# Kernel optimization log

Hardware: AMD Instinct MI355X
Metric: run time of the kernel (lower is better)

## Reference

```python
import jax, jax.numpy as jnp
import numpy as np

D_MODEL = 1024
N_HEADS = 16
HEAD_DIM = D_MODEL // N_HEADS


def setup_inputs() -> dict:
    key = jax.random.key(0)
    k_x, k_q, k_k, k_v = jax.random.split(key, 4)
    B, S = 2, 2048
    x = jax.random.normal(k_x, (B, S, D_MODEL), dtype=jnp.float32)
    # nn.Linear weights stored as [out, in]; we apply x @ W.T
    scale = 1.0 / np.sqrt(D_MODEL)
    W_q = jax.random.uniform(k_q, (D_MODEL, D_MODEL), jnp.float32, -scale, scale)
    W_k = jax.random.uniform(k_k, (D_MODEL, D_MODEL), jnp.float32, -scale, scale)
    W_v = jax.random.uniform(k_v, (D_MODEL, D_MODEL), jnp.float32, -scale, scale)
    return {"x": x, "W_q": W_q, "W_k": W_k, "W_v": W_v}


def reference(x, W_q, W_k, W_v):
    B, S, D = x.shape
    H, Hd = N_HEADS, HEAD_DIM
    # QKV projections (Linear with no bias): x @ W.T
    Q = (x @ W_q.T).reshape(B, S, H, Hd).transpose(0, 2, 1, 3)  # [B,H,S,Hd]
    K = (x @ W_k.T).reshape(B, S, H, Hd).transpose(0, 2, 1, 3)
    V = (x @ W_v.T).reshape(B, S, H, Hd).transpose(0, 2, 1, 3)
    scores = jnp.einsum("bhqd,bhkd->bhqk", Q, K) / jnp.sqrt(jnp.float32(Hd))
    attn = jax.nn.softmax(scores, axis=-1)
    out = jnp.einsum("bhqk,bhkd->bhqd", attn, V)  # [B,H,S,Hd]
    return out.transpose(0, 2, 1, 3).reshape(B, S, H * Hd)
```

## Files before the change

### kernel.cpp

```cpp
#include <hip/hip_runtime.h>
#include <stdint.h>


typedef __bf16 bf16x8 __attribute__((ext_vector_type(8)));
typedef __bf16 bf16x4 __attribute__((ext_vector_type(4)));
typedef __bf16 bf16x2 __attribute__((ext_vector_type(2)));
typedef float  f32x2  __attribute__((ext_vector_type(2)));
typedef float  f32x4  __attribute__((ext_vector_type(4)));
typedef float  f32x16 __attribute__((ext_vector_type(16)));

#define D_MODEL 1024
#define SEQ     2048
#define NHEAD   16
#define HDIM    64
#define BS      4096

__device__ __forceinline__ void load_lds16(const void* g, void* lds) {
  __builtin_amdgcn_global_load_lds(
      (__attribute__((address_space(1))) void*)(uintptr_t)g,
      (__attribute__((address_space(3))) void*)(uintptr_t)lds,
      16, 0, 0);
}

#if __has_builtin(__builtin_amdgcn_exp2f)
#define EXP2F(x) __builtin_amdgcn_exp2f(x)
#else
#define EXP2F(x) __expf(0.6931471805599453f * (x))
#endif

__device__ __forceinline__ uint32_t pack_bf16_pair(float a, float b) {
  f32x2 f = {a, b};
  union { bf16x2 h; uint32_t u; } r;
  r.h = __builtin_convertvector(f, bf16x2);
  return r.u;
}

#define NX4 1048576
#define NW4 262144
__global__ void cvt_all(const float* __restrict__ x,  const float* __restrict__ wq,
                        const float* __restrict__ wk, const float* __restrict__ wv,
                        __bf16* __restrict__ xb,  __bf16* __restrict__ wqb,
                        __bf16* __restrict__ wkb, __bf16* __restrict__ wvb) {
  int i = blockIdx.x * blockDim.x + threadIdx.x;
  const float* in; __bf16* out; int j;
  if (i < NX4)                { in = x;  out = xb;  j = i; }
  else if (i < NX4 + NW4)     { in = wq; out = wqb; j = i - NX4; }
  else if (i < NX4 + 2*NW4)   { in = wk; out = wkb; j = i - NX4 - NW4; }
  else                        { in = wv; out = wvb; j = i - NX4 - 2*NW4; }
  float4 v = ((const float4*)in)[j];
  bf16x4 o;
  o[0] = (__bf16)v.x; o[1] = (__bf16)v.y;
  o[2] = (__bf16)v.z; o[3] = (__bf16)v.w;
  ((bf16x4*)out)[j] = o;
}

__global__ __launch_bounds__(256) void qkv_gemm(
    const __bf16* __restrict__ X,
    const __bf16* __restrict__ Wq, const __bf16* __restrict__ Wk,
    const __bf16* __restrict__ Wv,
    __bf16* __restrict__ Qb, __bf16* __restrict__ Kb, __bf16* __restrict__ Vt) {
  __shared__ __bf16 As[128 * 32];
  __shared__ __bf16 Bs[128 * 32];

  const __bf16* W = (blockIdx.z == 0) ? Wq : (blockIdx.z == 1) ? Wk : Wv;

  const int t    = threadIdx.x;
  const int wv   = t >> 6;
  const int lane = t & 63;
  const int l15  = lane & 15;
  const int quad = lane >> 4;
  const int m0   = blockIdx.y * 128;
  const int n0   = blockIdx.x * 128;
  const int wm   = (wv >> 1) * 64;
  const int wn   = (wv & 1) * 64;

  f32x4 acc[4][4] = {};

  for (int it = 0; it < 32; ++it) {
    const int k0 = it * 32;
#pragma unroll
    for (int p = 0; p < 2; ++p) {
      const int c   = p * 256 + t;
      const int row = c >> 2;
      const int ko  = (c & 3) * 8;
      const unsigned lb = (unsigned)((p * 256 + wv * 64) * 16);
      load_lds16(X + (size_t)(m0 + row) * D_MODEL + k0 + ko, (char*)As + lb);
      load_lds16(W + (size_t)(n0 + row) * D_MODEL + k0 + ko, (char*)Bs + lb);
    }
    __syncthreads();

    bf16x8 af[4], bfb[4];
#pragma unroll
    for (int i = 0; i < 4; ++i)
      af[i] = *(const bf16x8*)&As[(wm + i * 16 + l15) * 32 + quad * 8];
#pragma unroll
    for (int j = 0; j < 4; ++j)
      bfb[j] = *(const bf16x8*)&Bs[(wn + j * 16 + l15) * 32 + quad * 8];
#pragma unroll
    for (int i = 0; i < 4; ++i)
#pragma unroll
      for (int j = 0; j < 4; ++j)
        acc[i][j] = __builtin_amdgcn_mfma_f32_16x16x32_bf16(af[i], bfb[j],
                                                            acc[i][j], 0, 0, 0);
    __syncthreads();
  }

  if (blockIdx.z != 2) {
    __bf16* Out = (blockIdx.z == 0) ? Qb : Kb;
    const float qs = (blockIdx.z == 0) ? 0.125f * 1.4426950408889634f : 1.0f;
#pragma unroll
    for (int i = 0; i < 4; ++i) {
      const int rg = m0 + wm + i * 16 + quad * 4;
#pragma unroll
      for (int j = 0; j < 4; ++j) {
        const int cg = n0 + wn + j * 16 + l15;
#pragma unroll
        for (int r2 = 0; r2 < 4; ++r2)
          Out[(size_t)(rg + r2) * D_MODEL + cg] = (__bf16)(acc[i][j][r2] * qs);
      }
    }
  } else {
#pragma unroll
    for (int i = 0; i < 4; ++i) {
      const int mg = m0 + wm + i * 16 + quad * 4;
#pragma unroll
      for (int j = 0; j < 4; ++j) {
        const int ng = n0 + wn + j * 16 + l15;
        bf16x4 v;
#pragma unroll
        for (int r2 = 0; r2 < 4; ++r2) v[r2] = (__bf16)acc[i][j][r2];
        *(bf16x4*)&Vt[(size_t)ng * BS + mg] = v;
      }
    }
  }
}

__global__ __launch_bounds__(256) void attn(
    const __bf16* __restrict__ Qb, const __bf16* __restrict__ Kb,
    const __bf16* __restrict__ Vt, float* __restrict__ out) {
  __shared__ __align__(16) char smem[16896];
  __bf16* Ks = (__bf16*)smem;
  __bf16* Vs = (__bf16*)(smem + 8192);
  float*  cmb = (float*)smem;

  const int t     = threadIdx.x;
  const int wv    = t >> 6;
  const int qgrp  = wv >> 1;
  const int ktile = wv & 1;
  const int lane  = t & 63;
  const int l31   = lane & 31;
  const int half  = lane >> 5;
  const int h     = blockIdx.y;
  const size_t bo = (size_t)blockIdx.z * SEQ;
  const int q0    = blockIdx.x * 64 + qgrp * 32;
  const int hd0   = h * HDIM;

  bf16x8 qf[4];
#pragma unroll
  for (int c = 0; c < 4; ++c)
    qf[c] = *(const bf16x8*)&Qb[(bo + q0 + l31) * D_MODEL + hd0 + c * 16 + half * 8];

  f32x2 lsum2 = {0.f, 0.f};
  f32x16 o_acc[2] = {};

  const int srow = ktile * 32 + l31;

  for (int kt = 0; kt < SEQ / 64; ++kt) {
    const int n0 = kt * 64;
#pragma unroll
    for (int p = 0; p < 2; ++p) {
      const int c   = p * 256 + t;
      const int row = c >> 3;
      const int cc  = (c & 7) ^ (row & 7);
      const unsigned lb = (unsigned)((p * 256 + wv * 64) * 16);
      load_lds16(Kb + (bo + n0 + row) * D_MODEL + hd0 + cc * 8, (char*)Ks + lb);
      load_lds16(Vt + (size_t)(hd0 + row) * BS + bo + n0 + cc * 8, (char*)Vs + lb);
    }
    __syncthreads();

    f32x16 st = {};
#pragma unroll
    for (int c = 0; c < 4; ++c) {
      const int pc = (2 * c + half) ^ (srow & 7);
      bf16x8 kf = *(const bf16x8*)&Ks[(srow * 8 + pc) * 8];
      st = __builtin_amdgcn_mfma_f32_32x32x16_bf16(kf, qf[c], st, 0, 0, 0);
    }

    uint32_t pk[8];
#pragma unroll
    for (int i = 0; i < 8; ++i) {
      float e0 = EXP2F(st[2 * i]);
      float e1 = EXP2F(st[2 * i + 1]);
      f32x2 e = {e0, e1};
      lsum2 += e;
      pk[i] = pack_bf16_pair(e0, e1);
    }

#pragma unroll
    for (int kc = 0; kc < 2; ++kc) {
      auto r02 = __builtin_amdgcn_permlane32_swap(pk[kc * 4 + 0], pk[kc * 4 + 2],
                                                  false, false);
      auto r13 = __builtin_amdgcn_permlane32_swap(pk[kc * 4 + 1], pk[kc * 4 + 3],
                                                  false, false);
      union { uint32_t u[4]; bf16x8 v; } pf;
      pf.u[0] = r02[0]; pf.u[1] = r13[0];
      pf.u[2] = r02[1]; pf.u[3] = r13[1];
#pragma unroll
      for (int dt = 0; dt < 2; ++dt) {
        const int row = dt * 32 + l31;
        const int pc  = (ktile * 4 + kc * 2 + half) ^ (row & 7);
        bf16x8 vf = *(const bf16x8*)&Vs[(row * 8 + pc) * 8];
        o_acc[dt] = __builtin_amdgcn_mfma_f32_32x32x16_bf16(vf, pf.v,
                                                            o_acc[dt], 0, 0, 0);
      }
    }
    __syncthreads();
  }

  float lsum = lsum2[0] + lsum2[1];

  if (ktile == 1) {
    float* p = cmb + (size_t)(qgrp * 64 + lane) * 33;
#pragma unroll
    for (int dt = 0; dt < 2; ++dt)
#pragma unroll
      for (int g = 0; g < 16; ++g) p[dt * 16 + g] = o_acc[dt][g];
    p[32] = lsum;
  }
  __syncthreads();
  if (ktile == 0) {
    const float* p = cmb + (size_t)(qgrp * 64 + lane) * 33;
#pragma unroll
    for (int dt = 0; dt < 2; ++dt)
#pragma unroll
      for (int g = 0; g < 16; ++g) o_acc[dt][g] += p[dt * 16 + g];
    lsum += p[32];
    lsum += __shfl_xor(lsum, 32);
    const float inv = 1.f / lsum;

    const size_t orow = (bo + q0 + l31) * D_MODEL + hd0;
#pragma unroll
    for (int dt = 0; dt < 2; ++dt)
#pragma unroll
      for (int g = 0; g < 4; ++g) {
        float4 v = make_float4(o_acc[dt][4 * g + 0] * inv, o_acc[dt][4 * g + 1] * inv,
                               o_acc[dt][4 * g + 2] * inv, o_acc[dt][4 * g + 3] * inv);
        *(float4*)&out[orow + dt * 32 + g * 8 + half * 4] = v;
      }
  }
}

extern "C" void kernel_launch(void* const* d_in, const int* in_sizes, int n_in,
                              void* d_out, int out_size, void* d_ws, size_t ws_size,
                              hipStream_t stream) {
  const float* x  = (const float*)d_in[0];
  const float* Wq = (const float*)d_in[1];
  const float* Wk = (const float*)d_in[2];
  const float* Wv = (const float*)d_in[3];
  float* out = (float*)d_out;

  char* ws = (char*)d_ws;
  __bf16* xb  = (__bf16*)(ws);
  __bf16* wqb = (__bf16*)(ws + (8u  << 20));
  __bf16* wkb = (__bf16*)(ws + (10u << 20));
  __bf16* wvb = (__bf16*)(ws + (12u << 20));
  __bf16* Qbf = (__bf16*)(ws + (14u << 20));
  __bf16* Kbf = (__bf16*)(ws + (22u << 20));
  __bf16* Vt  = (__bf16*)(ws + (30u << 20));

  cvt_all<<<(NX4 + 3 * NW4) / 256, 256, 0, stream>>>(x, Wq, Wk, Wv,
                                                     xb, wqb, wkb, wvb);

  qkv_gemm<<<dim3(8, 32, 3), 256, 0, stream>>>(xb, wqb, wkb, wvb, Qbf, Kbf, Vt);

  attn<<<dim3(SEQ / 64, NHEAD, 2), 256, 0, stream>>>(Qbf, Kbf, Vt, out);
}
```

Before: 162.3 us.

## Fuse conversion, QKV GEMM and attention into one cooperative persistent kernel

Merges the three launches (fp32→bf16 conversion, QKV projection GEMM, flash attention) into one cooperative kernel of 1024 blocks that uses grid-wide syncs between phases. Conversion is strided across all blocks, the first 768 blocks run the GEMM tiles, and every block then runs one attention tile. The aim is to remove the launch gaps and tail effects between kernels. In exchange it adds grid barriers, leaves a quarter of the blocks idle during the GEMM phase, and falls back to the old three-kernel path if the cooperative launch fails.

Measured after the change: 590.1 us. +263.6%, slower.

```diff
diff --git a/kernel.cpp b/kernel.cpp
--- a/kernel.cpp
+++ b/kernel.cpp
@@ -1,5 +1,8 @@
 #include <hip/hip_runtime.h>
+#include <hip/hip_cooperative_groups.h>
 #include <stdint.h>
+
+namespace cg = cooperative_groups;
 
 
 typedef __bf16 bf16x8 __attribute__((ext_vector_type(8)));
@@ -14,6 +17,8 @@
 #define NHEAD   16
 #define HDIM    64
 #define BS      4096
+#define NX4 1048576
+#define NW4 262144
 
 __device__ __forceinline__ void load_lds16(const void* g, void* lds) {
   __builtin_amdgcn_global_load_lds(
@@ -35,42 +40,41 @@
   return r.u;
 }
 
-#define NX4 1048576
-#define NW4 262144
-__global__ void cvt_all(const float* __restrict__ x,  const float* __restrict__ wq,
-                        const float* __restrict__ wk, const float* __restrict__ wv,
-                        __bf16* __restrict__ xb,  __bf16* __restrict__ wqb,
-                        __bf16* __restrict__ wkb, __bf16* __restrict__ wvb) {
-  int i = blockIdx.x * blockDim.x + threadIdx.x;
-  const float* in; __bf16* out; int j;
-  if (i < NX4)                { in = x;  out = xb;  j = i; }
-  else if (i < NX4 + NW4)     { in = wq; out = wqb; j = i - NX4; }
-  else if (i < NX4 + 2*NW4)   { in = wk; out = wkb; j = i - NX4 - NW4; }
-  else                        { in = wv; out = wvb; j = i - NX4 - 2*NW4; }
+
+__device__ __forceinline__ void cvt_item(
+    int i, const float* __restrict__ x,  const float* __restrict__ wq,
+    const float* __restrict__ wk, const float* __restrict__ wv,
+    __bf16* __restrict__ xb,  __bf16* __restrict__ wqb,
+    __bf16* __restrict__ wkb, __bf16* __restrict__ wvb) {
+  const float* in; __bf16* o; int j;
+  if (i < NX4)                { in = x;  o = xb;  j = i; }
+  else if (i < NX4 + NW4)     { in = wq; o = wqb; j = i - NX4; }
+  else if (i < NX4 + 2*NW4)   { in = wk; o = wkb; j = i - NX4 - NW4; }
+  else                        { in = wv; o = wvb; j = i - NX4 - 2*NW4; }
   float4 v = ((const float4*)in)[j];
-  bf16x4 o;
-  o[0] = (__bf16)v.x; o[1] = (__bf16)v.y;
-  o[2] = (__bf16)v.z; o[3] = (__bf16)v.w;
-  ((bf16x4*)out)[j] = o;
-}
-
-__global__ __launch_bounds__(256) void qkv_gemm(
+  bf16x4 ov;
+  ov[0] = (__bf16)v.x; ov[1] = (__bf16)v.y;
+  ov[2] = (__bf16)v.z; ov[3] = (__bf16)v.w;
+  ((bf16x4*)o)[j] = ov;
+}
+
+__device__ __forceinline__ void gemm_block(
+    int bx, int by, int bz, int t, char* smem,
     const __bf16* __restrict__ X,
     const __bf16* __restrict__ Wq, const __bf16* __restrict__ Wk,
     const __bf16* __restrict__ Wv,
     __bf16* __restrict__ Qb, __bf16* __restrict__ Kb, __bf16* __restrict__ Vt) {
-  __shared__ __bf16 As[128 * 32];
-  __shared__ __bf16 Bs[128 * 32];
-
-  const __bf16* W = (blockIdx.z == 0) ? Wq : (blockIdx.z == 1) ? Wk : Wv;
-
-  const int t    = threadIdx.x;
+  __bf16* As = (__bf16*)smem;
+  __bf16* Bs = (__bf16*)(smem + 8192);
+
+  const __bf16* W = (bz == 0) ? Wq : (bz == 1) ? Wk : Wv;
+
   const int wv   = t >> 6;
   const int lane = t & 63;
   const int l15  = lane & 15;
   const int quad = lane >> 4;
-  const int m0   = blockIdx.y * 128;
-  const int n0   = blockIdx.x * 128;
+  const int m0   = by * 128;
+  const int n0   = bx * 128;
   const int wm   = (wv >> 1) * 64;
   const int wn   = (wv & 1) * 64;
 
@@ -105,9 +109,9 @@
     __syncthreads();
   }
 
-  if (blockIdx.z != 2) {
-    __bf16* Out = (blockIdx.z == 0) ? Qb : Kb;
-    const float qs = (blockIdx.z == 0) ? 0.125f * 1.4426950408889634f : 1.0f;
+  if (bz != 2) {
+    __bf16* Out = (bz == 0) ? Qb : Kb;
+    const float qs = (bz == 0) ? 0.125f * 1.4426950408889634f : 1.0f;
 #pragma unroll
     for (int i = 0; i < 4; ++i) {
       const int rg = m0 + wm + i * 16 + quad * 4;
@@ -135,24 +139,22 @@
   }
 }
 
-__global__ __launch_bounds__(256) void attn(
+__device__ __forceinline__ void attn_block(
+    int bx, int h, int bz, int t, char* smem,
     const __bf16* __restrict__ Qb, const __bf16* __restrict__ Kb,
     const __bf16* __restrict__ Vt, float* __restrict__ out) {
-  __shared__ __align__(16) char smem[16896];
   __bf16* Ks = (__bf16*)smem;
   __bf16* Vs = (__bf16*)(smem + 8192);
   float*  cmb = (float*)smem;
 
-  const int t     = threadIdx.x;
   const int wv    = t >> 6;
   const int qgrp  = wv >> 1;
   const int ktile = wv & 1;
   const int lane  = t & 63;
   const int l31   = lane & 31;
   const int half  = lane >> 5;
-  const int h     = blockIdx.y;
-  const size_t bo = (size_t)blockIdx.z * SEQ;
-  const int q0    = blockIdx.x * 64 + qgrp * 32;
+  const size_t bo = (size_t)bz * SEQ;
+  const int q0    = bx * 64 + qgrp * 32;
   const int hd0   = h * HDIM;
 
   bf16x8 qf[4];
@@ -171,10 +173,10 @@
     for (int p = 0; p < 2; ++p) {
       const int c   = p * 256 + t;
       const int row = c >> 3;
-      const int cc  = (c & 7) ^ (row & 7);
+      const int ccx = (c & 7) ^ (row & 7);
       const unsigned lb = (unsigned)((p * 256 + wv * 64) * 16);
-      load_lds16(Kb + (bo + n0 + row) * D_MODEL + hd0 + cc * 8, (char*)Ks + lb);
-      load_lds16(Vt + (size_t)(hd0 + row) * BS + bo + n0 + cc * 8, (char*)Vs + lb);
+      load_lds16(Kb + (bo + n0 + row) * D_MODEL + hd0 + ccx * 8, (char*)Ks + lb);
+      load_lds16(Vt + (size_t)(hd0 + row) * BS + bo + n0 + ccx * 8, (char*)Vs + lb);
     }
     __syncthreads();
 
@@ -250,6 +252,65 @@
   }
 }
 
+__global__ __launch_bounds__(256, 4) void fused(
+    const float* __restrict__ x,  const float* __restrict__ wq,
+    const float* __restrict__ wk, const float* __restrict__ wv,
+    __bf16* __restrict__ xb,  __bf16* __restrict__ wqb,
+    __bf16* __restrict__ wkb, __bf16* __restrict__ wvb,
+    __bf16* __restrict__ Qb, __bf16* __restrict__ Kb, __bf16* __restrict__ Vt,
+    float* __restrict__ out) {
+  __shared__ __align__(16) char smem[16896];
+  cg::grid_group grid = cg::this_grid();
+
+  const int t = threadIdx.x;
+  const unsigned flat = blockIdx.x + 32u * blockIdx.y + 512u * blockIdx.z;
+
+  {
+    int i = (int)(flat * 256u) + t;
+#pragma unroll
+    for (int itc = 0; itc < 7; ++itc, i += 262144)
+      cvt_item(i, x, wq, wk, wv, xb, wqb, wkb, wvb);
+  }
+  __threadfence();
+  grid.sync();
+
+  if (flat < 768u) {
+    const int bz = (int)(flat >> 8);
+    const int r  = (int)(flat & 255u);
+    gemm_block(r & 7, r >> 3, bz, t, smem, xb, wqb, wkb, wvb, Qb, Kb, Vt);
+  }
+  __threadfence();
+  grid.sync();
+
+  attn_block(blockIdx.x, blockIdx.y, blockIdx.z, t, smem, Qb, Kb, Vt, out);
+}
+
+__global__ void cvt_all(const float* __restrict__ x,  const float* __restrict__ wq,
+                        const float* __restrict__ wk, const float* __restrict__ wv,
+                        __bf16* __restrict__ xb,  __bf16* __restrict__ wqb,
+                        __bf16* __restrict__ wkb, __bf16* __restrict__ wvb) {
+  int i = blockIdx.x * blockDim.x + threadIdx.x;
+  cvt_item(i, x, wq, wk, wv, xb, wqb, wkb, wvb);
+}
+
+__global__ __launch_bounds__(256) void qkv_gemm(
+    const __bf16* __restrict__ X,
+    const __bf16* __restrict__ Wq, const __bf16* __restrict__ Wk,
+    const __bf16* __restrict__ Wv,
+    __bf16* __restrict__ Qb, __bf16* __restrict__ Kb, __bf16* __restrict__ Vt) {
+  __shared__ __align__(16) char smem[16384];
+  gemm_block(blockIdx.x, blockIdx.y, blockIdx.z, threadIdx.x, smem,
+             X, Wq, Wk, Wv, Qb, Kb, Vt);
+}
+
+__global__ __launch_bounds__(256) void attn(
+    const __bf16* __restrict__ Qb, const __bf16* __restrict__ Kb,
+    const __bf16* __restrict__ Vt, float* __restrict__ out) {
+  __shared__ __align__(16) char smem[16896];
+  attn_block(blockIdx.x, blockIdx.y, blockIdx.z, threadIdx.x, smem,
+             Qb, Kb, Vt, out);
+}
+
 extern "C" void kernel_launch(void* const* d_in, const int* in_sizes, int n_in,
                               void* d_out, int out_size, void* d_ws, size_t ws_size,
                               hipStream_t stream) {
@@ -268,10 +329,20 @@
   __bf16* Kbf = (__bf16*)(ws + (22u << 20));
   __bf16* Vt  = (__bf16*)(ws + (30u << 20));
 
-  cvt_all<<<(NX4 + 3 * NW4) / 256, 256, 0, stream>>>(x, Wq, Wk, Wv,
-                                                     xb, wqb, wkb, wvb);
-
-  qkv_gemm<<<dim3(8, 32, 3), 256, 0, stream>>>(xb, wqb, wkb, wvb, Qbf, Kbf, Vt);
-
-  attn<<<dim3(SEQ / 64, NHEAD, 2), 256, 0, stream>>>(Qbf, Kbf, Vt, out);
-}
+  void* args[12];
+  args[0]  = (void*)&x;   args[1]  = (void*)&Wq;  args[2]  = (void*)&Wk;
+  args[3]  = (void*)&Wv;  args[4]  = (void*)&xb;  args[5]  = (void*)&wqb;
+  args[6]  = (void*)&wkb; args[7]  = (void*)&wvb; args[8]  = (void*)&Qbf;
+  args[9]  = (void*)&Kbf; args[10] = (void*)&Vt;  args[11] = (void*)&out;
+
+  hipError_t e = hipLaunchCooperativeKernel(
+      (const void*)fused, dim3(32, 16, 2), dim3(256, 1, 1), args, 0, stream);
+
+  if (e != hipSuccess) {
+    cvt_all<<<(NX4 + 3 * NW4) / 256, 256, 0, stream>>>(x, Wq, Wk, Wv,
+                                                       xb, wqb, wkb, wvb);
+    qkv_gemm<<<dim3(8, 32, 3), 256, 0, stream>>>(xb, wqb, wkb, wvb,
+                                                 Qbf, Kbf, Vt);
+    attn<<<dim3(32, 16, 2), 256, 0, stream>>>(Qbf, Kbf, Vt, out);
+  }
+}
```
